# Kernel optimization log

Hardware: AMD Instinct MI355X
Metric: run time of the kernel (lower is better)

## Reference

```python
import jax, jax.numpy as jnp
import numpy as np

N, E, F, C, H, L, ED = 100000, 1600000, 128, 16, 2, 2, 4
EPS = 1e-5
NEG_SLOPE = 0.2


def setup_inputs() -> dict:
    key = jax.random.key(0)
    ks = jax.random.split(key, 32)
    s = 0.1
    inp = {
        "x": jax.random.normal(ks[0], (N, F), dtype=jnp.float32),
        "edge_index": jax.random.randint(ks[1], (2, E), 0, N, dtype=jnp.int64),
        "edge_attr": jax.random.uniform(ks[2], (E, ED), dtype=jnp.float32),
        "embed_W": jax.random.normal(ks[3], (F, C)) * s,
        "embed_b": jnp.zeros((C,), jnp.float32),
        "ln0_w": jnp.ones((C,), jnp.float32),
        "ln0_b": jnp.zeros((C,), jnp.float32),
        "Wl": jax.random.normal(ks[4], (L, C, H * C)) * s,
        "bl": jnp.zeros((L, H * C), jnp.float32),
        "Wr": jax.random.normal(ks[5], (L, C, H * C)) * s,
        "br": jnp.zeros((L, H * C), jnp.float32),
        "We": jax.random.normal(ks[6], (L, ED, H * C)) * s,
        "att": jax.random.normal(ks[7], (L, H, C)) * s,
        "gat_b": jnp.zeros((L, H * C), jnp.float32),
        "n1_w": jnp.ones((L, H * C), jnp.float32),
        "n1_b": jnp.zeros((L, H * C), jnp.float32),
        "lin_W": jax.random.normal(ks[8], (L, H * C, C)) * s,
        "lin_b": jnp.zeros((L, C), jnp.float32),
        "n2_w": jnp.ones((L, C), jnp.float32),
        "n2_b": jnp.zeros((L, C), jnp.float32),
    }
    return inp


def _node_ln(v, w, b):
    # torch.nn.LayerNorm over the feature dim (per node)
    mu = v.mean(-1, keepdims=True)
    var = ((v - mu) ** 2).mean(-1, keepdims=True)
    return (v - mu) / jnp.sqrt(var + EPS) * w + b


def _graph_ln(v, w, b):
    # PyG norm.LayerNorm(mode='graph'): normalize over ALL nodes and channels
    mu = v.mean()
    vc = v - mu
    return vc / jnp.sqrt((vc * vc).mean() + EPS) * w + b


def reference(x, edge_index, edge_attr, embed_W, embed_b, ln0_w, ln0_b,
              Wl, bl, Wr, br, We, att, gat_b, n1_w, n1_b,
              lin_W, lin_b, n2_w, n2_b):
    n = x.shape[0]
    heads, c = att.shape[1], att.shape[2]
    layers = Wl.shape[0]

    # node embedding MLP (dropout = identity in eval)
    h = jax.nn.relu(_node_ln(x @ embed_W + embed_b, ln0_w, ln0_b))

    # add self-loops (fill_value=0.0 -> zero edge features, lin_edge has no bias)
    loop = jnp.arange(n)
    src = jnp.concatenate([edge_index[0], loop])
    dst = jnp.concatenate([edge_index[1], loop])

    hs = [h]
    for i in range(layers):
        xl = (h @ Wl[i] + bl[i]).reshape(n, heads, c)   # source transform (x_j)
        xr = (h @ Wr[i] + br[i]).reshape(n, heads, c)   # target transform (x_i)
        ew = (edge_attr @ We[i]).reshape(-1, heads, c)
        ew = jnp.concatenate([ew, jnp.zeros((n, heads, c), ew.dtype)], axis=0)

        msg = xl[src] + xr[dst] + ew                      # [E+N, H, C]
        logits = jnp.einsum('ehc,hc->eh', jax.nn.leaky_relu(msg, NEG_SLOPE), att[i])
        m = jax.ops.segment_max(logits, dst, num_segments=n)
        ex = jnp.exp(logits - m[dst])
        den = jax.ops.segment_sum(ex, dst, num_segments=n)
        alpha = ex / den[dst]                             # segment softmax over dst

        g = jax.ops.segment_sum(alpha[..., None] * xl[src], dst, num_segments=n)
        g = g.reshape(n, heads * c) + gat_b[i]

        g = jax.nn.relu(_graph_ln(g, n1_w[i], n1_b[i]))
        g = g @ lin_W[i] + lin_b[i]
        g = _graph_ln(g, n2_w[i], n2_b[i])
        h = jax.nn.relu(g + h)                            # residual + relu
        hs.append(h)

    # JumpingKnowledge mode='max': elementwise max over layer outputs
    return jnp.max(jnp.stack(hs, axis=0), axis=0)
```

## Files before the change

kernel.cpp:

```cpp
#include <hip/hip_runtime.h>

#define N_NODES 100000
#define N_EDGES 1600000
#define NF 128
#define NC 16
#define NH 2
#define HC 32
#define NL 2
#define NED 4
#define EPS 1e-5f
#define NEG 0.2f
#define NBUCK 196
#define P1_CHUNK 4096
#define P1_BLKS ((N_EDGES + P1_CHUNK - 1) / P1_CHUNK)
#define AGG_BLKS ((N_NODES + 31) / 32)
#define MID_BLKS ((N_NODES + 15) / 16)

typedef __attribute__((ext_vector_type(2))) float f32x2;

__device__ __forceinline__ unsigned short f2bf(float f) {
    unsigned int u = __float_as_uint(f);
    u += 0x7fffu + ((u >> 16) & 1u);
    return (unsigned short)(u >> 16);
}
__device__ __forceinline__ float bf2f(unsigned short u) {
    return __uint_as_float(((unsigned int)u) << 16);
}
__device__ __forceinline__ unsigned int pack_bf2(float a, float b) {
    return (unsigned int)f2bf(a) | ((unsigned int)f2bf(b) << 16);
}
__device__ __forceinline__ float bflo(int u) {
    return __uint_as_float(((unsigned int)u) << 16);
}
__device__ __forceinline__ float bfhi(int u) {
    return __uint_as_float(((unsigned int)u) & 0xffff0000u);
}
__device__ __forceinline__ f32x2 sp2(float v) { f32x2 r; r.x = v; r.y = v; return r; }
__device__ __forceinline__ void bf4_gather(const unsigned short* base, unsigned boff,
                                           f32x2& p01, f32x2& p23) {
    int2 v = *(const int2*)((const char*)base + boff);
    p01.x = bflo(v.x); p01.y = bfhi(v.x);
    p23.x = bflo(v.y); p23.y = bfhi(v.y);
}

__global__ __launch_bounds__(256) void k_embed(
    const float* __restrict__ x, const float* __restrict__ W,
    const float* __restrict__ b, const float* __restrict__ lnw,
    const float* __restrict__ lnb, float* __restrict__ h, float* __restrict__ jk)
{
    __shared__ __align__(16) float WsT[NC][NF + 4];
    __shared__ __align__(16) float xs[16][NF + 4];
    const int t = threadIdx.x;
    for (int i = t; i < NF * NC; i += 256) {
        int f = i >> 4, c = i & 15;
        WsT[c][f] = W[i];
    }
    const int n0 = blockIdx.x * 16;
    const float4* x4 = (const float4*)x;
    for (int i = t; i < 16 * (NF / 4); i += 256) {
        int r = i >> 5, f4 = i & 31;
        int n = n0 + r;
        float4 v = (n < N_NODES) ? x4[(size_t)n * (NF / 4) + f4]
                                 : make_float4(0.f, 0.f, 0.f, 0.f);
        *(float4*)&xs[r][f4 * 4] = v;
    }
    __syncthreads();
    const int r = t >> 4;
    const int c = t & 15;
    const int n = n0 + r;
    float acc = b[c];
#pragma unroll
    for (int f4 = 0; f4 < NF / 4; ++f4) {
        float4 xv = *(const float4*)&xs[r][f4 * 4];
        float4 wv = *(const float4*)&WsT[c][f4 * 4];
        acc += xv.x * wv.x + xv.y * wv.y + xv.z * wv.z + xv.w * wv.w;
    }
    float s = acc;
    for (int m = 8; m >= 1; m >>= 1) s += __shfl_xor(s, m, 16);
    float mu = s * (1.f / 16.f);
    float d = acc - mu;
    float v = d * d;
    for (int m = 8; m >= 1; m >>= 1) v += __shfl_xor(v, m, 16);
    float inv = rsqrtf(v * (1.f / 16.f) + EPS);
    float out = fmaxf(d * inv * lnw[c] + lnb[c], 0.f);
    if (n < N_NODES) {
        h[(size_t)n * NC + c]  = out;
        jk[(size_t)n * NC + c] = out;
    }
}

__global__ __launch_bounds__(256) void k_bhist(
    const int* __restrict__ dst, int* __restrict__ bcnt)
{
    __shared__ int hist[256];
    const int t = threadIdx.x;
    hist[t] = 0;
    __syncthreads();
    const int e0 = blockIdx.x * P1_CHUNK;
    const int cnt = min(P1_CHUNK, N_EDGES - e0);
    for (int i = t; i < cnt; i += 256)
        atomicAdd(&hist[dst[e0 + i] >> 9], 1);
    __syncthreads();
    if (hist[t] > 0) atomicAdd(&bcnt[t], hist[t]);
}

__global__ __launch_bounds__(256) void k_bscan(
    const int* __restrict__ bcnt, int* __restrict__ bbase, int* __restrict__ bcur)
{
    __shared__ int tmp[256];
    const int t = threadIdx.x;
    int v0 = bcnt[t];
    tmp[t] = v0;
    __syncthreads();
    for (int off = 1; off < 256; off <<= 1) {
        int v = (t >= off) ? tmp[t - off] : 0;
        __syncthreads();
        tmp[t] += v;
        __syncthreads();
    }
    int excl = tmp[t] - v0;
    bbase[t] = excl;
    bcur[t]  = excl;
    if (t == 255) bbase[256] = tmp[t];
}

__global__ __launch_bounds__(256) void k_pass1(
    const int* __restrict__ src, const int* __restrict__ dst,
    const float4* __restrict__ ea4, int* __restrict__ bcur,
    int4* __restrict__ tmp_rec)
{
    __shared__ int hist[256];
    __shared__ int gbase[256];
    __shared__ int lcur[256];
    const int t = threadIdx.x;
    const int e0 = blockIdx.x * P1_CHUNK;
    const int cnt = min(P1_CHUNK, N_EDGES - e0);
    hist[t] = 0; lcur[t] = 0;
    __syncthreads();
    for (int i = t; i < cnt; i += 256)
        atomicAdd(&hist[dst[e0 + i] >> 9], 1);
    __syncthreads();
    {
        int c = hist[t];
        gbase[t] = (c > 0) ? atomicAdd(&bcur[t], c) : 0;
    }
    __syncthreads();
    for (int i = t; i < cnt; i += 256) {
        int e = e0 + i;
        int d = dst[e];
        int s = src[e];
        float4 ea = ea4[e];
        int b = d >> 9;
        int lpos = atomicAdd(&lcur[b], 1);
        tmp_rec[gbase[b] + lpos] = make_int4(s, d,
                                             (int)pack_bf2(ea.x, ea.y),
                                             (int)pack_bf2(ea.z, ea.w));
    }
}

__global__ __launch_bounds__(256) void k_pass2(
    const int* __restrict__ bbase, const int4* __restrict__ tmp_rec,
    int* __restrict__ offsets, int4* __restrict__ csr)
{
    __shared__ int hist[512];
    __shared__ int cur[512];
    __shared__ int scanbuf[256];
    const int b = blockIdx.x, t = threadIdx.x;
    const int ebeg = bbase[b], eend = bbase[b + 1];
    hist[t] = 0; hist[t + 256] = 0;
    __syncthreads();
    for (int i = ebeg + t; i < eend; i += 256)
        atomicAdd(&hist[tmp_rec[i].y & 511], 1);
    __syncthreads();
    int a0 = hist[2 * t], a1 = hist[2 * t + 1];
    int pair = a0 + a1;
    scanbuf[t] = pair;
    __syncthreads();
    for (int off = 1; off < 256; off <<= 1) {
        int v = (t >= off) ? scanbuf[t - off] : 0;
        __syncthreads();
        scanbuf[t] += v;
        __syncthreads();
    }
    int ex2 = scanbuf[t] - pair;
    cur[2 * t]     = ex2;
    cur[2 * t + 1] = ex2 + a0;
    __syncthreads();
    const int n0 = b * 512;
#pragma unroll
    for (int k = 0; k < 2; ++k) {
        int i = t + k * 256;
        int n = n0 + i;
        if (n < N_NODES) offsets[n] = ebeg + cur[i];
    }
    if (b == NBUCK - 1 && t == 0) offsets[N_NODES] = N_EDGES;
    __syncthreads();
    for (int i = ebeg + t; i < eend; i += 256) {
        int4 rec = tmp_rec[i];
        int pos = ebeg + atomicAdd(&cur[rec.y & 511], 1);
        csr[pos] = rec;
    }
}

__global__ __launch_bounds__(256) void k_trans(
    const float* __restrict__ h, const float* __restrict__ Wl, const float* __restrict__ bl,
    const float* __restrict__ Wr, const float* __restrict__ br,
    unsigned short* __restrict__ xl, unsigned short* __restrict__ xr)
{
    __shared__ float Wls[NC * HC], Wrs[NC * HC];
    __shared__ float hs[8][NC + 1];
    const int t = threadIdx.x;
    for (int i = t; i < NC * HC; i += 256) { Wls[i] = Wl[i]; Wrs[i] = Wr[i]; }
    const int n0 = blockIdx.x * 8;
    for (int i = t; i < 8 * NC; i += 256) {
        int r = i >> 4, c = i & 15;
        int n = n0 + r;
        hs[r][c] = (n < N_NODES) ? h[(size_t)n * NC + c] : 0.f;
    }
    __syncthreads();
    const int r = t >> 5;
    const int j = t & 31;
    const int n = n0 + r;
    float al = bl[j], ar = br[j];
#pragma unroll
    for (int c = 0; c < NC; ++c) {
        float hv = hs[r][c];
        al += hv * Wls[c * HC + j];
        ar += hv * Wrs[c * HC + j];
    }
    if (n < N_NODES) {
        xl[(size_t)n * HC + j] = f2bf(al);
        xr[(size_t)n * HC + j] = f2bf(ar);
    }
}

__global__ __launch_bounds__(256) void k_agg(
    const int* __restrict__ offsets, const int4* __restrict__ csr,
    const float* __restrict__ We, const float* __restrict__ att,
    const float* __restrict__ gat_b,
    const unsigned short* __restrict__ xl, const unsigned short* __restrict__ xr,
    float* __restrict__ g, float2* __restrict__ part)
{
    __shared__ float Wes[NED * HC];
    __shared__ float atts[HC], gbs[HC];
    const int t = threadIdx.x;
    if (t < NED * HC) Wes[t] = We[t];
    if (t < HC) { atts[t] = att[t]; gbs[t] = gat_b[t]; }
    __syncthreads();
    const int grp = t >> 3;
    const int l   = t & 7;
    const int d = blockIdx.x * 32 + grp;
    f32x2 gv01 = sp2(0.f), gv23 = sp2(0.f);
    if (d < N_NODES) {
        const int c0 = l << 2;
        f32x2 a01; a01.x = atts[c0];     a01.y = atts[c0 + 1];
        f32x2 a23; a23.x = atts[c0 + 2]; a23.y = atts[c0 + 3];
        f32x2 w0a, w0b, w1a, w1b, w2a, w2b, w3a, w3b;
        w0a.x = Wes[c0];          w0a.y = Wes[c0 + 1];
        w0b.x = Wes[c0 + 2];      w0b.y = Wes[c0 + 3];
        w1a.x = Wes[HC + c0];     w1a.y = Wes[HC + c0 + 1];
        w1b.x = Wes[HC + c0 + 2]; w1b.y = Wes[HC + c0 + 3];
        w2a.x = Wes[2 * HC + c0];     w2a.y = Wes[2 * HC + c0 + 1];
        w2b.x = Wes[2 * HC + c0 + 2]; w2b.y = Wes[2 * HC + c0 + 3];
        w3a.x = Wes[3 * HC + c0];     w3a.y = Wes[3 * HC + c0 + 1];
        w3b.x = Wes[3 * HC + c0 + 2]; w3b.y = Wes[3 * HC + c0 + 3];
        const unsigned jb = (unsigned)(l << 3);
        f32x2 xld01, xld23, xrd01, xrd23;
        bf4_gather(xl, ((unsigned)d << 6) + jb, xld01, xld23);
        bf4_gather(xr, ((unsigned)d << 6) + jb, xrd01, xrd23);
        f32x2 m01 = xld01 + xrd01, m23 = xld23 + xrd23;
        m01.x = fmaxf(m01.x, NEG * m01.x); m01.y = fmaxf(m01.y, NEG * m01.y);
        m23.x = fmaxf(m23.x, NEG * m23.x); m23.y = fmaxf(m23.y, NEG * m23.y);
        float p = m01.x * a01.x + m01.y * a01.y + m23.x * a23.x + m23.y * a23.y;
        p += __shfl_xor(p, 1);
        p += __shfl_xor(p, 2);
        float eh = __expf(p);
        f32x2 acc01 = sp2(eh) * xld01, acc23 = sp2(eh) * xld23;
        float den = eh;
        const int base = offsets[d];
        const int deg  = offsets[d + 1] - base;
        int k = 0;
        for (; k + 4 <= deg; k += 4) {
            const int b0 = base + k;
            const int4 r0 = csr[b0],     r1 = csr[b0 + 1];
            const int4 r2 = csr[b0 + 2], r3 = csr[b0 + 3];
            f32x2 x0a, x0b, x1a, x1b, x2a, x2b, x3a, x3b;
            bf4_gather(xl, ((unsigned)r0.x << 6) + jb, x0a, x0b);
            bf4_gather(xl, ((unsigned)r1.x << 6) + jb, x1a, x1b);
            bf4_gather(xl, ((unsigned)r2.x << 6) + jb, x2a, x2b);
            bf4_gather(xl, ((unsigned)r3.x << 6) + jb, x3a, x3b);
            f32x2 m0a = x0a + xrd01, m0b = x0b + xrd23;
            f32x2 m1a = x1a + xrd01, m1b = x1b + xrd23;
            f32x2 m2a = x2a + xrd01, m2b = x2b + xrd23;
            f32x2 m3a = x3a + xrd01, m3b = x3b + xrd23;
            m0a += sp2(bflo(r0.z)) * w0a; m0b += sp2(bflo(r0.z)) * w0b;
            m1a += sp2(bflo(r1.z)) * w0a; m1b += sp2(bflo(r1.z)) * w0b;
            m2a += sp2(bflo(r2.z)) * w0a; m2b += sp2(bflo(r2.z)) * w0b;
            m3a += sp2(bflo(r3.z)) * w0a; m3b += sp2(bflo(r3.z)) * w0b;
            m0a += sp2(bfhi(r0.z)) * w1a; m0b += sp2(bfhi(r0.z)) * w1b;
            m1a += sp2(bfhi(r1.z)) * w1a; m1b += sp2(bfhi(r1.z)) * w1b;
            m2a += sp2(bfhi(r2.z)) * w1a; m2b += sp2(bfhi(r2.z)) * w1b;
            m3a += sp2(bfhi(r3.z)) * w1a; m3b += sp2(bfhi(r3.z)) * w1b;
            m0a += sp2(bflo(r0.w)) * w2a; m0b += sp2(bflo(r0.w)) * w2b;
            m1a += sp2(bflo(r1.w)) * w2a; m1b += sp2(bflo(r1.w)) * w2b;
            m2a += sp2(bflo(r2.w)) * w2a; m2b += sp2(bflo(r2.w)) * w2b;
            m3a += sp2(bflo(r3.w)) * w2a; m3b += sp2(bflo(r3.w)) * w2b;
            m0a += sp2(bfhi(r0.w)) * w3a; m0b += sp2(bfhi(r0.w)) * w3b;
            m1a += sp2(bfhi(r1.w)) * w3a; m1b += sp2(bfhi(r1.w)) * w3b;
            m2a += sp2(bfhi(r2.w)) * w3a; m2b += sp2(bfhi(r2.w)) * w3b;
            m3a += sp2(bfhi(r3.w)) * w3a; m3b += sp2(bfhi(r3.w)) * w3b;
            m0a.x = fmaxf(m0a.x, NEG * m0a.x); m0a.y = fmaxf(m0a.y, NEG * m0a.y);
            m0b.x = fmaxf(m0b.x, NEG * m0b.x); m0b.y = fmaxf(m0b.y, NEG * m0b.y);
            m1a.x = fmaxf(m1a.x, NEG * m1a.x); m1a.y = fmaxf(m1a.y, NEG * m1a.y);
            m1b.x = fmaxf(m1b.x, NEG * m1b.x); m1b.y = fmaxf(m1b.y, NEG * m1b.y);
            m2a.x = fmaxf(m2a.x, NEG * m2a.x); m2a.y = fmaxf(m2a.y, NEG * m2a.y);
            m2b.x = fmaxf(m2b.x, NEG * m2b.x); m2b.y = fmaxf(m2b.y, NEG * m2b.y);
            m3a.x = fmaxf(m3a.x, NEG * m3a.x); m3a.y = fmaxf(m3a.y, NEG * m3a.y);
            m3b.x = fmaxf(m3b.x, NEG * m3b.x); m3b.y = fmaxf(m3b.y, NEG * m3b.y);
            float p0 = m0a.x * a01.x + m0a.y * a01.y + m0b.x * a23.x + m0b.y * a23.y;
            float p1 = m1a.x * a01.x + m1a.y * a01.y + m1b.x * a23.x + m1b.y * a23.y;
            float p2 = m2a.x * a01.x + m2a.y * a01.y + m2b.x * a23.x + m2b.y * a23.y;
            float p3 = m3a.x * a01.x + m3a.y * a01.y + m3b.x * a23.x + m3b.y * a23.y;
            p0 += __shfl_xor(p0, 1); p1 += __shfl_xor(p1, 1);
            p2 += __shfl_xor(p2, 1); p3 += __shfl_xor(p3, 1);
            p0 += __shfl_xor(p0, 2); p1 += __shfl_xor(p1, 2);
            p2 += __shfl_xor(p2, 2); p3 += __shfl_xor(p3, 2);
            const float ee0 = __expf(p0), ee1 = __expf(p1);
            const float ee2 = __expf(p2), ee3 = __expf(p3);
            acc01 += sp2(ee0) * x0a; acc23 += sp2(ee0) * x0b;
            acc01 += sp2(ee1) * x1a; acc23 += sp2(ee1) * x1b;
            acc01 += sp2(ee2) * x2a; acc23 += sp2(ee2) * x2b;
            acc01 += sp2(ee3) * x3a; acc23 += sp2(ee3) * x3b;
            den += ee0 + ee1 + ee2 + ee3;
        }
        for (; k < deg; ++k) {
            const int4 r = csr[base + k];
            f32x2 xa, xb;
            bf4_gather(xl, ((unsigned)r.x << 6) + jb, xa, xb);
            f32x2 ma = xa + xrd01, mb = xb + xrd23;
            ma += sp2(bflo(r.z)) * w0a; mb += sp2(bflo(r.z)) * w0b;
            ma += sp2(bfhi(r.z)) * w1a; mb += sp2(bfhi(r.z)) * w1b;
            ma += sp2(bflo(r.w)) * w2a; mb += sp2(bflo(r.w)) * w2b;
            ma += sp2(bfhi(r.w)) * w3a; mb += sp2(bfhi(r.w)) * w3b;
            ma.x = fmaxf(ma.x, NEG * ma.x); ma.y = fmaxf(ma.y, NEG * ma.y);
            mb.x = fmaxf(mb.x, NEG * mb.x); mb.y = fmaxf(mb.y, NEG * mb.y);
            float p = ma.x * a01.x + ma.y * a01.y + mb.x * a23.x + mb.y * a23.y;
            p += __shfl_xor(p, 1);
            p += __shfl_xor(p, 2);
            const float ee = __expf(p);
            acc01 += sp2(ee) * xa; acc23 += sp2(ee) * xb;
            den += ee;
        }
        const float invd = 1.f / den;
        gv01.x = acc01.x * invd + gbs[c0];
        gv01.y = acc01.y * invd + gbs[c0 + 1];
        gv23.x = acc23.x * invd + gbs[c0 + 2];
        gv23.y = acc23.y * invd + gbs[c0 + 3];
        float4 wv; wv.x = gv01.x; wv.y = gv01.y; wv.z = gv23.x; wv.w = gv23.y;
        *(float4*)&g[(size_t)d * HC + c0] = wv;
    }
    float s  = gv01.x + gv01.y + gv23.x + gv23.y;
    float ss = gv01.x * gv01.x + gv01.y * gv01.y + gv23.x * gv23.x + gv23.y * gv23.y;
    for (int m = 32; m >= 1; m >>= 1) { s += __shfl_xor(s, m); ss += __shfl_xor(ss, m); }
    __shared__ float sr[4], ssr[4];
    const int w = t >> 6;
    if ((t & 63) == 0) { sr[w] = s; ssr[w] = ss; }
    __syncthreads();
    if (t == 0) part[blockIdx.x] = make_float2(sr[0] + sr[1] + sr[2] + sr[3],
                                               ssr[0] + ssr[1] + ssr[2] + ssr[3]);
}

__global__ __launch_bounds__(256) void k_red(
    const float2* __restrict__ part, int n, double* __restrict__ out)
{
    const int t = threadIdx.x;
    double s = 0.0, ss = 0.0;
    for (int i = t; i < n; i += 256) {
        float2 p = part[i];
        s += (double)p.x; ss += (double)p.y;
    }
    for (int m = 32; m >= 1; m >>= 1) { s += __shfl_xor(s, m); ss += __shfl_xor(ss, m); }
    __shared__ double sr[4], ssr[4];
    const int w = t >> 6;
    if ((t & 63) == 0) { sr[w] = s; ssr[w] = ss; }
    __syncthreads();
    if (t == 0) {
        out[0] = sr[0] + sr[1] + sr[2] + sr[3];
        out[1] = ssr[0] + ssr[1] + ssr[2] + ssr[3];
    }
}

__global__ __launch_bounds__(256) void k_mid(
    const float* __restrict__ g,
    const float* __restrict__ n1w, const float* __restrict__ n1b,
    const float* __restrict__ linW, const float* __restrict__ linb,
    const double* __restrict__ stats1, float* __restrict__ g2,
    float2* __restrict__ part)
{
    __shared__ float Ws[HC * NC];
    __shared__ float rs[16][HC + 1];
    const int t = threadIdx.x;
    for (int i = t; i < HC * NC; i += 256) Ws[i] = linW[i];
    const double cnt = (double)N_NODES * HC;
    const double mud = stats1[0] / cnt;
    const float mu  = (float)mud;
    const float var = (float)(stats1[1] / cnt - mud * mud);
    const float inv = rsqrtf(var + EPS);
    const int n0 = blockIdx.x * 16;
    for (int i = t; i < 16 * HC; i += 256) {
        int r = i >> 5, j = i & 31;
        int n = n0 + r;
        float v = (n < N_NODES) ? g[(size_t)n * HC + j] : mu;
        v = (v - mu) * inv * n1w[j] + n1b[j];
        rs[r][j] = fmaxf(v, 0.f);
    }
    __syncthreads();
    const int r = t >> 4, c = t & 15;
    const int n = n0 + r;
    float acc = linb[c];
#pragma unroll
    for (int j = 0; j < HC; ++j) acc += rs[r][j] * Ws[j * NC + c];
    float val = (n < N_NODES) ? acc : 0.f;
    if (n < N_NODES) g2[(size_t)n * NC + c] = acc;
    float s = val, ss = val * val;
    for (int m = 32; m >= 1; m >>= 1) { s += __shfl_xor(s, m); ss += __shfl_xor(ss, m); }
    __shared__ float sr[4], ssr[4];
    const int w = t >> 6;
    if ((t & 63) == 0) { sr[w] = s; ssr[w] = ss; }
    __syncthreads();
    if (t == 0) part[blockIdx.x] = make_float2(sr[0] + sr[1] + sr[2] + sr[3],
                                               ssr[0] + ssr[1] + ssr[2] + ssr[3]);
}

__global__ __launch_bounds__(256) void k_ftrans(
    const float* __restrict__ g2, const float* __restrict__ n2w,
    const float* __restrict__ n2b, const double* __restrict__ stats2,
    float* __restrict__ h, float* __restrict__ jk,
    const float* __restrict__ Wl, const float* __restrict__ bl,
    const float* __restrict__ Wr, const float* __restrict__ br,
    unsigned short* __restrict__ xl, unsigned short* __restrict__ xr)
{
    __shared__ float Wls[NC * HC], Wrs[NC * HC];
    __shared__ float hs[8][NC + 1];
    const int t = threadIdx.x;
    for (int i = t; i < NC * HC; i += 256) { Wls[i] = Wl[i]; Wrs[i] = Wr[i]; }
    const double cnt = (double)N_NODES * NC;
    const double mud = stats2[0] / cnt;
    const float mu  = (float)mud;
    const float var = (float)(stats2[1] / cnt - mud * mud);
    const float inv = rsqrtf(var + EPS);
    const int n0 = blockIdx.x * 8;
    if (t < 8 * NC) {
        int r = t >> 4, c = t & 15;
        int n = n0 + r;
        if (n < N_NODES) {
            size_t idx = (size_t)n * NC + c;
            float v = (g2[idx] - mu) * inv * n2w[c] + n2b[c];
            float hn = fmaxf(v + h[idx], 0.f);
            h[idx] = hn;
            jk[idx] = fmaxf(jk[idx], hn);
            hs[r][c] = hn;
        } else hs[r][c] = 0.f;
    }
    __syncthreads();
    const int r = t >> 5;
    const int j = t & 31;
    const int n = n0 + r;
    float al = bl[j], ar = br[j];
#pragma unroll
    for (int c = 0; c < NC; ++c) {
        float hv = hs[r][c];
        al += hv * Wls[c * HC + j];
        ar += hv * Wrs[c * HC + j];
    }
    if (n < N_NODES) {
        xl[(size_t)n * HC + j] = f2bf(al);
        xr[(size_t)n * HC + j] = f2bf(ar);
    }
}

__global__ __launch_bounds__(256) void k_final(
    const float* __restrict__ g2, const float* __restrict__ n2w,
    const float* __restrict__ n2b, const double* __restrict__ stats2,
    float* __restrict__ h, float* __restrict__ jk)
{
    const int i = blockIdx.x * 256 + threadIdx.x;
    if (i >= N_NODES * NC) return;
    const double cnt = (double)N_NODES * NC;
    const double mud = stats2[0] / cnt;
    const float mu  = (float)mud;
    const float var = (float)(stats2[1] / cnt - mud * mud);
    const float inv = rsqrtf(var + EPS);
    const int c = i & (NC - 1);
    float v = (g2[i] - mu) * inv * n2w[c] + n2b[c];
    float hn = fmaxf(v + h[i], 0.f);
    h[i] = hn;
    jk[i] = fmaxf(jk[i], hn);
}

extern "C" void kernel_launch(void* const* d_in, const int* in_sizes, int n_in,
                              void* d_out, int out_size, void* d_ws, size_t ws_size,
                              hipStream_t stream)
{
    const float* x     = (const float*)d_in[0];
    const int*   eidx  = (const int*)d_in[1];
    const float* eattr = (const float*)d_in[2];
    const float* embW  = (const float*)d_in[3];
    const float* embB  = (const float*)d_in[4];
    const float* ln0w  = (const float*)d_in[5];
    const float* ln0b  = (const float*)d_in[6];
    const float* Wl    = (const float*)d_in[7];
    const float* bl    = (const float*)d_in[8];
    const float* Wr    = (const float*)d_in[9];
    const float* br    = (const float*)d_in[10];
    const float* We    = (const float*)d_in[11];
    const float* att   = (const float*)d_in[12];
    const float* gatb  = (const float*)d_in[13];
    const float* n1w   = (const float*)d_in[14];
    const float* n1b   = (const float*)d_in[15];
    const float* linW  = (const float*)d_in[16];
    const float* linb  = (const float*)d_in[17];
    const float* n2w   = (const float*)d_in[18];
    const float* n2b   = (const float*)d_in[19];
    float* out = (float*)d_out;

    char* ws = (char*)d_ws;
    double* stats = (double*)ws;
    char* p = ws + 1024;
    int* bcnt = (int*)p; p += 1024;
    int* bbase = (int*)p; p += 4096;
    int* bcur  = (int*)p; p += 1024;
    int* offsets = (int*)p; p += (size_t)(N_NODES + 64) * 4;
    float* g = (float*)p; p += (size_t)N_NODES * HC * 4;
    int4* csr = (int4*)p; p += (size_t)N_EDGES * 16;
    int4* tmp_rec = (int4*)p;
    char* q = p;
    p += (size_t)N_EDGES * 16;
    float* hq = (float*)q; q += (size_t)N_NODES * NC * 4;
    unsigned short* xlq = (unsigned short*)q; q += (size_t)N_NODES * HC * 2;
    unsigned short* xrq = (unsigned short*)q; q += (size_t)N_NODES * HC * 2;
    float* g2q = (float*)q;
    float2* part1 = (float2*)p; p += (size_t)MID_BLKS * 8;
    float2* part2 = (float2*)p; p += (size_t)MID_BLKS * 8;

    const int* srcp = eidx;
    const int* dstp = eidx + N_EDGES;

    hipMemsetAsync(bcnt, 0, 1024, stream);
    k_bhist<<<P1_BLKS, 256, 0, stream>>>(dstp, bcnt);
    k_bscan<<<1, 256, 0, stream>>>(bcnt, bbase, bcur);
    k_pass1<<<P1_BLKS, 256, 0, stream>>>(srcp, dstp, (const float4*)eattr,
                                         bcur, tmp_rec);
    k_pass2<<<NBUCK, 256, 0, stream>>>(bbase, tmp_rec, offsets, csr);

    k_embed<<<(N_NODES + 15) / 16, 256, 0, stream>>>(x, embW, embB, ln0w, ln0b, hq, out);

    k_trans<<<(N_NODES + 7) / 8, 256, 0, stream>>>(hq, Wl, bl, Wr, br, xlq, xrq);
    k_agg<<<AGG_BLKS, 256, 0, stream>>>(
        offsets, csr, We, att, gatb, xlq, xrq, g, part1);
    k_red<<<1, 256, 0, stream>>>(part1, AGG_BLKS, stats);
    k_mid<<<MID_BLKS, 256, 0, stream>>>(
        g, n1w, n1b, linW, linb, stats, g2q, part2);
    k_red<<<1, 256, 0, stream>>>(part2, MID_BLKS, stats + 2);
    k_ftrans<<<(N_NODES + 7) / 8, 256, 0, stream>>>(
        g2q, n2w, n2b, stats + 2, hq, out,
        Wl + NC * HC, bl + HC, Wr + NC * HC, br + HC, xlq, xrq);
    k_agg<<<AGG_BLKS, 256, 0, stream>>>(
        offsets, csr, We + NED * HC, att + HC, gatb + HC, xlq, xrq, g, part1);
    k_red<<<1, 256, 0, stream>>>(part1, AGG_BLKS, stats);
    k_mid<<<MID_BLKS, 256, 0, stream>>>(
        g, n1w + HC, n1b + HC, linW + HC * NC, linb + NC, stats, g2q, part2);
    k_red<<<1, 256, 0, stream>>>(part2, MID_BLKS, stats + 2);
    k_final<<<(N_NODES * NC + 255) / 256, 256, 0, stream>>>(
        g2q, n2w + NC, n2b + NC, stats + 2, hq, out);
}
```

Before: 423.6 us.

## Replace per-block partial stats and reduce kernels with double atomics; widen pass2 blocks

Removes the four single-block k_red launches by having k_agg and k_mid atomically add their per-block sums into double-precision stats slots, which are zeroed by a new memset. k_pass2 now runs 512 threads per block so each thread handles one node slot and edge loops stride by 512. In k_agg, the four neighbour gathers in the unrolled loop are issued together before unpacking to improve memory-level parallelism. The trade-off is atomic contention on two doubles from thousands of blocks and a reduction order that is no longer deterministic.

```diff
diff --git a/kernel.cpp b/kernel.cpp
--- a/kernel.cpp
+++ b/kernel.cpp
@@ -36,11 +36,12 @@
     return __uint_as_float(((unsigned int)u) & 0xffff0000u);
 }
 __device__ __forceinline__ f32x2 sp2(float v) { f32x2 r; r.x = v; r.y = v; return r; }
-__device__ __forceinline__ void bf4_gather(const unsigned short* base, unsigned boff,
-                                           f32x2& p01, f32x2& p23) {
-    int2 v = *(const int2*)((const char*)base + boff);
+__device__ __forceinline__ void bf4_unpack(int2 v, f32x2& p01, f32x2& p23) {
     p01.x = bflo(v.x); p01.y = bfhi(v.x);
     p23.x = bflo(v.y); p23.y = bfhi(v.y);
+}
+__device__ __forceinline__ int2 ld8(const unsigned short* base, unsigned boff) {
+    return *(const int2*)((const char*)base + boff);
 }
 
 __global__ __launch_bounds__(256) void k_embed(
@@ -158,7 +159,7 @@
     }
 }
 
-__global__ __launch_bounds__(256) void k_pass2(
+__global__ __launch_bounds__(512) void k_pass2(
     const int* __restrict__ bbase, const int4* __restrict__ tmp_rec,
     int* __restrict__ offsets, int4* __restrict__ csr)
 {
@@ -167,35 +168,37 @@
     __shared__ int scanbuf[256];
     const int b = blockIdx.x, t = threadIdx.x;
     const int ebeg = bbase[b], eend = bbase[b + 1];
-    hist[t] = 0; hist[t + 256] = 0;
-    __syncthreads();
-    for (int i = ebeg + t; i < eend; i += 256)
+    hist[t] = 0;
+    __syncthreads();
+    for (int i = ebeg + t; i < eend; i += 512)
         atomicAdd(&hist[tmp_rec[i].y & 511], 1);
     __syncthreads();
-    int a0 = hist[2 * t], a1 = hist[2 * t + 1];
-    int pair = a0 + a1;
-    scanbuf[t] = pair;
+    int a0 = 0, a1 = 0, pair = 0;
+    if (t < 256) {
+        a0 = hist[2 * t]; a1 = hist[2 * t + 1];
+        pair = a0 + a1;
+        scanbuf[t] = pair;
+    }
     __syncthreads();
     for (int off = 1; off < 256; off <<= 1) {
-        int v = (t >= off) ? scanbuf[t - off] : 0;
+        int v = (t < 256 && t >= off) ? scanbuf[t - off] : 0;
         __syncthreads();
-        scanbuf[t] += v;
+        if (t < 256) scanbuf[t] += v;
         __syncthreads();
     }
-    int ex2 = scanbuf[t] - pair;
-    cur[2 * t]     = ex2;
-    cur[2 * t + 1] = ex2 + a0;
-    __syncthreads();
-    const int n0 = b * 512;
-#pragma unroll
-    for (int k = 0; k < 2; ++k) {
-        int i = t + k * 256;
-        int n = n0 + i;
-        if (n < N_NODES) offsets[n] = ebeg + cur[i];
-    }
-    if (b == NBUCK - 1 && t == 0) offsets[N_NODES] = N_EDGES;
-    __syncthreads();
-    for (int i = ebeg + t; i < eend; i += 256) {
+    if (t < 256) {
+        int ex2 = scanbuf[t] - pair;
+        cur[2 * t]     = ex2;
+        cur[2 * t + 1] = ex2 + a0;
+    }
+    __syncthreads();
+    {
+        int n = b * 512 + t;
+        if (n < N_NODES) offsets[n] = ebeg + cur[t];
+        if (b == NBUCK - 1 && t == 0) offsets[N_NODES] = N_EDGES;
+    }
+    __syncthreads();
+    for (int i = ebeg + t; i < eend; i += 512) {
         int4 rec = tmp_rec[i];
         int pos = ebeg + atomicAdd(&cur[rec.y & 511], 1);
         csr[pos] = rec;
@@ -234,12 +237,20 @@
     }
 }
 
+#define EDGE_MSG(RA, RB, RZ, RW)                                              \
+    RA += sp2(bflo(RZ)) * w0a; RB += sp2(bflo(RZ)) * w0b;                     \
+    RA += sp2(bfhi(RZ)) * w1a; RB += sp2(bfhi(RZ)) * w1b;                     \
+    RA += sp2(bflo(RW)) * w2a; RB += sp2(bflo(RW)) * w2b;                     \
+    RA += sp2(bfhi(RW)) * w3a; RB += sp2(bfhi(RW)) * w3b;                     \
+    RA.x = fmaxf(RA.x, NEG * RA.x); RA.y = fmaxf(RA.y, NEG * RA.y);           \
+    RB.x = fmaxf(RB.x, NEG * RB.x); RB.y = fmaxf(RB.y, NEG * RB.y);
+
 __global__ __launch_bounds__(256) void k_agg(
     const int* __restrict__ offsets, const int4* __restrict__ csr,
     const float* __restrict__ We, const float* __restrict__ att,
     const float* __restrict__ gat_b,
     const unsigned short* __restrict__ xl, const unsigned short* __restrict__ xr,
-    float* __restrict__ g, float2* __restrict__ part)
+    float* __restrict__ g, double* __restrict__ outstats)
 {
     __shared__ float Wes[NED * HC];
     __shared__ float atts[HC], gbs[HC];
@@ -266,8 +277,8 @@
         w3b.x = Wes[3 * HC + c0 + 2]; w3b.y = Wes[3 * HC + c0 + 3];
         const unsigned jb = (unsigned)(l << 3);
         f32x2 xld01, xld23, xrd01, xrd23;
-        bf4_gather(xl, ((unsigned)d << 6) + jb, xld01, xld23);
-        bf4_gather(xr, ((unsigned)d << 6) + jb, xrd01, xrd23);
+        bf4_unpack(ld8(xl, ((unsigned)d << 6) + jb), xld01, xld23);
+        bf4_unpack(ld8(xr, ((unsigned)d << 6) + jb), xrd01, xrd23);
         f32x2 m01 = xld01 + xrd01, m23 = xld23 + xrd23;
         m01.x = fmaxf(m01.x, NEG * m01.x); m01.y = fmaxf(m01.y, NEG * m01.y);
         m23.x = fmaxf(m23.x, NEG * m23.x); m23.y = fmaxf(m23.y, NEG * m23.y);
@@ -284,39 +295,21 @@
             const int b0 = base + k;
             const int4 r0 = csr[b0],     r1 = csr[b0 + 1];
             const int4 r2 = csr[b0 + 2], r3 = csr[b0 + 3];
+            const int2 v0 = ld8(xl, ((unsigned)r0.x << 6) + jb);
+            const int2 v1 = ld8(xl, ((unsigned)r1.x << 6) + jb);
+            const int2 v2 = ld8(xl, ((unsigned)r2.x << 6) + jb);
+            const int2 v3 = ld8(xl, ((unsigned)r3.x << 6) + jb);
             f32x2 x0a, x0b, x1a, x1b, x2a, x2b, x3a, x3b;
-            bf4_gather(xl, ((unsigned)r0.x << 6) + jb, x0a, x0b);
-            bf4_gather(xl, ((unsigned)r1.x << 6) + jb, x1a, x1b);
-            bf4_gather(xl, ((unsigned)r2.x << 6) + jb, x2a, x2b);
-            bf4_gather(xl, ((unsigned)r3.x << 6) + jb, x3a, x3b);
+            bf4_unpack(v0, x0a, x0b); bf4_unpack(v1, x1a, x1b);
+            bf4_unpack(v2, x2a, x2b); bf4_unpack(v3, x3a, x3b);
             f32x2 m0a = x0a + xrd01, m0b = x0b + xrd23;
             f32x2 m1a = x1a + xrd01, m1b = x1b + xrd23;
             f32x2 m2a = x2a + xrd01, m2b = x2b + xrd23;
             f32x2 m3a = x3a + xrd01, m3b = x3b + xrd23;
-            m0a += sp2(bflo(r0.z)) * w0a; m0b += sp2(bflo(r0.z)) * w0b;
-            m1a += sp2(bflo(r1.z)) * w0a; m1b += sp2(bflo(r1.z)) * w0b;
-            m2a += sp2(bflo(r2.z)) * w0a; m2b += sp2(bflo(r2.z)) * w0b;
-            m3a += sp2(bflo(r3.z)) * w0a; m3b += sp2(bflo(r3.z)) * w0b;
-            m0a += sp2(bfhi(r0.z)) * w1a; m0b += sp2(bfhi(r0.z)) * w1b;
-            m1a += sp2(bfhi(r1.z)) * w1a; m1b += sp2(bfhi(r1.z)) * w1b;
-            m2a += sp2(bfhi(r2.z)) * w1a; m2b += sp2(bfhi(r2.z)) * w1b;
-            m3a += sp2(bfhi(r3.z)) * w1a; m3b += sp2(bfhi(r3.z)) * w1b;
-            m0a += sp2(bflo(r0.w)) * w2a; m0b += sp2(bflo(r0.w)) * w2b;
-            m1a += sp2(bflo(r1.w)) * w2a; m1b += sp2(bflo(r1.w)) * w2b;
-            m2a += sp2(bflo(r2.w)) * w2a; m2b += sp2(bflo(r2.w)) * w2b;
-            m3a += sp2(bflo(r3.w)) * w2a; m3b += sp2(bflo(r3.w)) * w2b;
-            m0a += sp2(bfhi(r0.w)) * w3a; m0b += sp2(bfhi(r0.w)) * w3b;
-            m1a += sp2(bfhi(r1.w)) * w3a; m1b += sp2(bfhi(r1.w)) * w3b;
-            m2a += sp2(bfhi(r2.w)) * w3a; m2b += sp2(bfhi(r2.w)) * w3b;
-            m3a += sp2(bfhi(r3.w)) * w3a; m3b += sp2(bfhi(r3.w)) * w3b;
-            m0a.x = fmaxf(m0a.x, NEG * m0a.x); m0a.y = fmaxf(m0a.y, NEG * m0a.y);
-            m0b.x = fmaxf(m0b.x, NEG * m0b.x); m0b.y = fmaxf(m0b.y, NEG * m0b.y);
-            m1a.x = fmaxf(m1a.x, NEG * m1a.x); m1a.y = fmaxf(m1a.y, NEG * m1a.y);
-            m1b.x = fmaxf(m1b.x, NEG * m1b.x); m1b.y = fmaxf(m1b.y, NEG * m1b.y);
-            m2a.x = fmaxf(m2a.x, NEG * m2a.x); m2a.y = fmaxf(m2a.y, NEG * m2a.y);
-            m2b.x = fmaxf(m2b.x, NEG * m2b.x); m2b.y = fmaxf(m2b.y, NEG * m2b.y);
-            m3a.x = fmaxf(m3a.x, NEG * m3a.x); m3a.y = fmaxf(m3a.y, NEG * m3a.y);
-            m3b.x = fmaxf(m3b.x, NEG * m3b.x); m3b.y = fmaxf(m3b.y, NEG * m3b.y);
+            EDGE_MSG(m0a, m0b, r0.z, r0.w)
+            EDGE_MSG(m1a, m1b, r1.z, r1.w)
+            EDGE_MSG(m2a, m2b, r2.z, r2.w)
+            EDGE_MSG(m3a, m3b, r3.z, r3.w)
             float p0 = m0a.x * a01.x + m0a.y * a01.y + m0b.x * a23.x + m0b.y * a23.y;
             float p1 = m1a.x * a01.x + m1a.y * a01.y + m1b.x * a23.x + m1b.y * a23.y;
             float p2 = m2a.x * a01.x + m2a.y * a01.y + m2b.x * a23.x + m2b.y * a23.y;
@@ -336,14 +329,9 @@
         for (; k < deg; ++k) {
             const int4 r = csr[base + k];
             f32x2 xa, xb;
-            bf4_gather(xl, ((unsigned)r.x << 6) + jb, xa, xb);
+            bf4_unpack(ld8(xl, ((unsigned)r.x << 6) + jb), xa, xb);
             f32x2 ma = xa + xrd01, mb = xb + xrd23;
-            ma += sp2(bflo(r.z)) * w0a; mb += sp2(bflo(r.z)) * w0b;
-            ma += sp2(bfhi(r.z)) * w1a; mb += sp2(bfhi(r.z)) * w1b;
-            ma += sp2(bflo(r.w)) * w2a; mb += sp2(bflo(r.w)) * w2b;
-            ma += sp2(bfhi(r.w)) * w3a; mb += sp2(bfhi(r.w)) * w3b;
-            ma.x = fmaxf(ma.x, NEG * ma.x); ma.y = fmaxf(ma.y, NEG * ma.y);
-            mb.x = fmaxf(mb.x, NEG * mb.x); mb.y = fmaxf(mb.y, NEG * mb.y);
+            EDGE_MSG(ma, mb, r.z, r.w)
             float p = ma.x * a01.x + ma.y * a01.y + mb.x * a23.x + mb.y * a23.y;
             p += __shfl_xor(p, 1);
             p += __shfl_xor(p, 2);
@@ -366,27 +354,9 @@
     const int w = t >> 6;
     if ((t & 63) == 0) { sr[w] = s; ssr[w] = ss; }
     __syncthreads();
-    if (t == 0) part[blockIdx.x] = make_float2(sr[0] + sr[1] + sr[2] + sr[3],
-                                               ssr[0] + ssr[1] + ssr[2] + ssr[3]);
-}
-
-__global__ __launch_bounds__(256) void k_red(
-    const float2* __restrict__ part, int n, double* __restrict__ out)
-{
-    const int t = threadIdx.x;
-    double s = 0.0, ss = 0.0;
-    for (int i = t; i < n; i += 256) {
-        float2 p = part[i];
-        s += (double)p.x; ss += (double)p.y;
-    }
-    for (int m = 32; m >= 1; m >>= 1) { s += __shfl_xor(s, m); ss += __shfl_xor(ss, m); }
-    __shared__ double sr[4], ssr[4];
-    const int w = t >> 6;
-    if ((t & 63) == 0) { sr[w] = s; ssr[w] = ss; }
-    __syncthreads();
     if (t == 0) {
-        out[0] = sr[0] + sr[1] + sr[2] + sr[3];
-        out[1] = ssr[0] + ssr[1] + ssr[2] + ssr[3];
+        atomicAdd(&outstats[0], (double)(sr[0] + sr[1] + sr[2] + sr[3]));
+        atomicAdd(&outstats[1], (double)(ssr[0] + ssr[1] + ssr[2] + ssr[3]));
     }
 }
 
@@ -395,7 +365,7 @@
     const float* __restrict__ n1w, const float* __restrict__ n1b,
     const float* __restrict__ linW, const float* __restrict__ linb,
     const double* __restrict__ stats1, float* __restrict__ g2,
-    float2* __restrict__ part)
+    double* __restrict__ outstats)
 {
     __shared__ float Ws[HC * NC];
     __shared__ float rs[16][HC + 1];
@@ -428,8 +398,10 @@
     const int w = t >> 6;
     if ((t & 63) == 0) { sr[w] = s; ssr[w] = ss; }
     __syncthreads();
-    if (t == 0) part[blockIdx.x] = make_float2(sr[0] + sr[1] + sr[2] + sr[3],
-                                               ssr[0] + ssr[1] + ssr[2] + ssr[3]);
+    if (t == 0) {
+        atomicAdd(&outstats[0], (double)(sr[0] + sr[1] + sr[2] + sr[3]));
+        atomicAdd(&outstats[1], (double)(ssr[0] + ssr[1] + ssr[2] + ssr[3]));
+    }
 }
 
 __global__ __launch_bounds__(256) void k_ftrans(
@@ -540,37 +512,32 @@
     unsigned short* xlq = (unsigned short*)q; q += (size_t)N_NODES * HC * 2;
     unsigned short* xrq = (unsigned short*)q; q += (size_t)N_NODES * HC * 2;
     float* g2q = (float*)q;
-    float2* part1 = (float2*)p; p += (size_t)MID_BLKS * 8;
-    float2* part2 = (float2*)p; p += (size_t)MID_BLKS * 8;
 
     const int* srcp = eidx;
     const int* dstp = eidx + N_EDGES;
 
     hipMemsetAsync(bcnt, 0, 1024, stream);
+    hipMemsetAsync(stats, 0, 64, stream);
     k_bhist<<<P1_BLKS, 256, 0, stream>>>(dstp, bcnt);
     k_bscan<<<1, 256, 0, stream>>>(bcnt, bbase, bcur);
     k_pass1<<<P1_BLKS, 256, 0, stream>>>(srcp, dstp, (const float4*)eattr,
                                          bcur, tmp_rec);
-    k_pass2<<<NBUCK, 256, 0, stream>>>(bbase, tmp_rec, offsets, csr);
+    k_pass2<<<NBUCK, 512, 0, stream>>>(bbase, tmp_rec, offsets, csr);
 
     k_embed<<<(N_NODES + 15) / 16, 256, 0, stream>>>(x, embW, embB, ln0w, ln0b, hq, out);
 
     k_trans<<<(N_NODES + 7) / 8, 256, 0, stream>>>(hq, Wl, bl, Wr, br, xlq, xrq);
     k_agg<<<AGG_BLKS, 256, 0, stream>>>(
-        offsets, csr, We, att, gatb, xlq, xrq, g, part1);
-    k_red<<<1, 256, 0, stream>>>(part1, AGG_BLKS, stats);
+        offsets, csr, We, att, gatb, xlq, xrq, g, stats + 0);
     k_mid<<<MID_BLKS, 256, 0, stream>>>(
-        g, n1w, n1b, linW, linb, stats, g2q, part2);
-    k_red<<<1, 256, 0, stream>>>(part2, MID_BLKS, stats + 2);
+        g, n1w, n1b, linW, linb, stats + 0, g2q, stats + 2);
     k_ftrans<<<(N_NODES + 7) / 8, 256, 0, stream>>>(
         g2q, n2w, n2b, stats + 2, hq, out,
         Wl + NC * HC, bl + HC, Wr + NC * HC, br + HC, xlq, xrq);
     k_agg<<<AGG_BLKS, 256, 0, stream>>>(
-        offsets, csr, We + NED * HC, att + HC, gatb + HC, xlq, xrq, g, part1);
-    k_red<<<1, 256, 0, stream>>>(part1, AGG_BLKS, stats);
+        offsets, csr, We + NED * HC, att + HC, gatb + HC, xlq, xrq, g, stats + 4);
     k_mid<<<MID_BLKS, 256, 0, stream>>>(
-        g, n1w + HC, n1b + HC, linW + HC * NC, linb + NC, stats, g2q, part2);
-    k_red<<<1, 256, 0, stream>>>(part2, MID_BLKS, stats + 2);
+        g, n1w + HC, n1b + HC, linW + HC * NC, linb + NC, stats + 4, g2q, stats + 6);
     k_final<<<(N_NODES * NC + 255) / 256, 256, 0, stream>>>(
-        g2q, n2w + NC, n2b + NC, stats + 2, hq, out);
-}
+        g2q, n2w + NC, n2b + NC, stats + 6, hq, out);
+}
```

Result: slower. 772.6 us (+82.4%).
